# Performance work log

Hardware: AMD Instinct MI355X
Metric: run time of the kernel (lower is better)

The kernel has to match this reference:

```python
import jax, jax.numpy as jnp
import numpy as np

EMBED_DIM = 1024
NUM_HEADS = 16
HEAD_DIM = EMBED_DIM // NUM_HEADS


def setup_inputs() -> dict:
    key = jax.random.key(0)
    ks = jax.random.split(key, 9)
    s = 1.0 / np.sqrt(EMBED_DIM)
    inp = {"x": jax.random.normal(ks[0], (2, 2048, EMBED_DIM), dtype=jnp.float32)}
    for i, name in enumerate(["q", "k", "v", "out"]):
        inp[f"W_{name}"] = jax.random.uniform(ks[1 + 2 * i], (EMBED_DIM, EMBED_DIM), jnp.float32, -s, s)
        inp[f"b_{name}"] = jax.random.uniform(ks[2 + 2 * i], (EMBED_DIM,), jnp.float32, -s, s)
    return inp


def _heads(x):
    # [B, S, D] -> [B, H, S, Dh]
    b, s, _ = x.shape
    return x.reshape(b, s, NUM_HEADS, HEAD_DIM).transpose(0, 2, 1, 3)


def reference(x, W_q, b_q, W_k, b_k, W_v, b_v, W_out, b_out):
    q = _heads(x @ W_q.T + b_q)
    k = _heads(x @ W_k.T + b_k)
    v = _heads(x @ W_v.T + b_v)
    scale = HEAD_DIM ** 0.5
    logits = jnp.einsum("bhqd,bhkd->bhqk", q, k) / scale  # [B,H,S,S]
    s = x.shape[1]
    causal = jnp.tril(jnp.ones((s, s), dtype=bool))
    logits = jnp.where(causal, logits, -jnp.inf)
    a = jax.nn.softmax(logits, axis=-1)
    o = jnp.einsum("bhqk,bhkd->bhqd", a, v)
    o = o.transpose(0, 2, 1, 3).reshape(x.shape[0], s, EMBED_DIM)
    return o @ W_out.T + b_out
```

## Files before the change

kernel.cpp:

```cpp
#include <hip/hip_runtime.h>
#include <hip/hip_bf16.h>

typedef __bf16 bf16_t;
typedef __bf16 bf16x8 __attribute__((ext_vector_type(8)));
typedef __bf16 bf16x4 __attribute__((ext_vector_type(4)));
typedef float  f32x4  __attribute__((ext_vector_type(4)));

#define MFMA16(a, b, c) __builtin_amdgcn_mfma_f32_16x16x32_bf16((a), (b), (c), 0, 0, 0)

constexpr int E  = 1024;
constexpr int S  = 2048;
constexpr int H  = 16;
constexpr int M  = 4096;

__device__ __forceinline__ void glds16(const bf16_t* src, bf16_t* dst) {
  __builtin_amdgcn_global_load_lds(
      (const __attribute__((address_space(1))) void*)src,
      (__attribute__((address_space(3))) void*)dst, 16, 0, 0);
}

template <int ROWS, int NT>
__device__ __forceinline__ void stage_tile(const bf16_t* g, int gld,
                                           bf16_t* lds, int tid) {
  const int w = tid >> 6, l = tid & 63;
#pragma unroll
  for (int i = 0; i < ROWS * 8 / NT; ++i) {
    const int c = i * NT + w * 64 + l;
    const int row = c >> 3;
    const int gch = (c & 7) ^ (row & 7);
    glds16(g + (size_t)row * gld + gch * 8, lds + (size_t)(i * NT + w * 64) * 8);
  }
}

__device__ __forceinline__ bf16x8 read_frag(const bf16_t* lds, int row, int kc) {
  return *(const bf16x8*)(lds + (size_t)((row << 3) + (kc ^ (row & 7))) * 8);
}

__global__ void cvt_all_kernel(const float* __restrict__ x,
                               const float* __restrict__ w0, const float* __restrict__ w1,
                               const float* __restrict__ w2, const float* __restrict__ w3,
                               bf16_t* __restrict__ xb,
                               bf16_t* __restrict__ o0, bf16_t* __restrict__ o1,
                               bf16_t* __restrict__ o2, bf16_t* __restrict__ o3) {
  const int bid = blockIdx.x;
  const float* s;
  bf16_t* d;
  int idx;
  if (bid < 4096) {
    s = x; d = xb; idx = bid * 256 + threadIdx.x;
  } else {
    const int seg = (bid - 4096) >> 10;
    s = seg == 0 ? w0 : seg == 1 ? w1 : seg == 2 ? w2 : w3;
    d = seg == 0 ? o0 : seg == 1 ? o1 : seg == 2 ? o2 : o3;
    idx = ((bid - 4096) & 1023) * 256 + threadIdx.x;
  }
  float4 v = ((const float4*)s)[idx];
  bf16x4 o;
  o[0] = (bf16_t)v.x; o[1] = (bf16_t)v.y; o[2] = (bf16_t)v.z; o[3] = (bf16_t)v.w;
  ((bf16x4*)d)[idx] = o;
}

__global__ __launch_bounds__(512, 2) void qkv8_kernel(
    const bf16_t* __restrict__ xb, const bf16_t* __restrict__ W3,
    const float* __restrict__ bq, const float* __restrict__ bk,
    const float* __restrict__ bv, bf16_t* __restrict__ QKb,
    bf16_t* __restrict__ VT) {
  __shared__ __align__(16) bf16_t As[2][256 * 64];
  __shared__ __align__(16) bf16_t Bs[2][192 * 64];
  const int tid = threadIdx.x;
  const int l = tid & 63, lq = l & 15, qd = l >> 4;
  const int w = tid >> 6, wm = w >> 2, wn = w & 3;

  const int wg = blockIdx.x;
  const int xcd = wg & 7, i5 = wg >> 3;
  const int region = xcd * 2 + (i5 >> 4);
  const int j = i5 & 15;
  const int bx = (region & 3) * 4 + (j & 3);
  const int by = (region >> 2) * 4 + (j >> 2);
  const int m0 = by * 256, n0 = bx * 192;

  const bf16_t* Ag = xb + (size_t)m0 * E;
  const bf16_t* Bg = W3 + (size_t)n0 * E;

  f32x4 acc[8][3];
#pragma unroll
  for (int mi = 0; mi < 8; ++mi)
#pragma unroll
    for (int n = 0; n < 3; ++n) acc[mi][n] = (f32x4){0.f, 0.f, 0.f, 0.f};

  stage_tile<256, 512>(Ag, E, As[0], tid);
  stage_tile<192, 512>(Bg, E, Bs[0], tid);
  __syncthreads();

#pragma unroll 1
  for (int g = 0; g < 16; ++g) {
    const int s = g & 1;
    const bf16_t* Al = As[s];
    const bf16_t* Bl = Bs[s];
    if (g < 15) {
      stage_tile<256, 512>(Ag + (g + 1) * 64, E, As[s ^ 1], tid);
      stage_tile<192, 512>(Bg + (g + 1) * 64, E, Bs[s ^ 1], tid);
    }
#pragma unroll
    for (int kk = 0; kk < 2; ++kk) {
      bf16x8 af[8], bfr[3];
#pragma unroll
      for (int jj = 0; jj < 8; ++jj)
        af[jj] = read_frag(Al, wm * 128 + jj * 16 + lq, kk * 4 + qd);
#pragma unroll
      for (int n = 0; n < 3; ++n)
        bfr[n] = read_frag(Bl, wn * 48 + n * 16 + lq, kk * 4 + qd);
#pragma unroll
      for (int jj = 0; jj < 8; ++jj)
#pragma unroll
        for (int n = 0; n < 3; ++n)
          acc[jj][n] = MFMA16(af[jj], bfr[n], acc[jj][n]);
    }
    __syncthreads();
  }

#pragma unroll
  for (int n = 0; n < 3; ++n) {
    const int col = n0 + wn * 48 + n * 16 + lq;
    const int mat = col >> 10, cc = col & 1023;
    const float bvv = (mat == 0 ? bq : mat == 1 ? bk : bv)[cc];
    if (mat < 2) {
      const float sc = (mat == 0) ? 0.18033688011112043f : 1.0f;
      bf16_t* Out = QKb + (size_t)mat * ((size_t)M * E);
#pragma unroll
      for (int mi = 0; mi < 8; ++mi)
#pragma unroll
        for (int r = 0; r < 4; ++r) {
          const int row = m0 + wm * 128 + mi * 16 + qd * 4 + r;
          Out[(size_t)row * E + cc] = (bf16_t)((acc[mi][n][r] + bvv) * sc);
        }
    } else {
      const int d = cc & 63, hh = cc >> 6;
#pragma unroll
      for (int mi = 0; mi < 8; ++mi) {
        const int row = m0 + wm * 128 + mi * 16 + qd * 4;
        const int bb_ = row >> 11;
        const int s_loc = row & (S - 1);
        const int sl = s_loc & 63, s0 = s_loc & ~63;
        const int a = sl >> 4, b4 = (sl >> 2) & 3;
        const int pb = (a >> 1) * 32 + b4 * 8 + (a & 1) * 4;
        bf16x4 vv;
#pragma unroll
        for (int r = 0; r < 4; ++r) vv[r] = (bf16_t)(acc[mi][n][r] + bvv);
        *(bf16x4*)&VT[((size_t)((bb_ * 16 + hh) * 64 + d)) * S + s0 + pb] = vv;
      }
    }
  }
}

__global__ __launch_bounds__(256) void oproj_gemm_kernel(
    const bf16_t* __restrict__ Ob, const bf16_t* __restrict__ wo,
    const float* __restrict__ bo, float* __restrict__ out) {
  __shared__ __align__(16) bf16_t As[64 * 64];
  __shared__ __align__(16) bf16_t Bs[128 * 64];
  const int tid = threadIdx.x;
  const int n0 = blockIdx.x * 128;
  const int m0 = blockIdx.y * 64;
  const int w = tid >> 6, l = tid & 63, lq = l & 15, qd = l >> 4;
  const int wr = (w >> 1) * 32, wc = (w & 1) * 64;

  f32x4 acc[2][4];
#pragma unroll
  for (int i = 0; i < 2; ++i)
#pragma unroll
    for (int j = 0; j < 4; ++j) acc[i][j] = (f32x4){0.f, 0.f, 0.f, 0.f};

  for (int kt = 0; kt < 16; ++kt) {
    __syncthreads();
    stage_tile<64, 256>(Ob + (size_t)m0 * E + kt * 64, E, As, tid);
    stage_tile<128, 256>(wo + (size_t)n0 * E + kt * 64, E, Bs, tid);
    __syncthreads();
#pragma unroll
    for (int ks = 0; ks < 2; ++ks) {
      bf16x8 af[2], bw[4];
#pragma unroll
      for (int mi = 0; mi < 2; ++mi)
        af[mi] = read_frag(As, wr + mi * 16 + lq, ks * 4 + qd);
#pragma unroll
      for (int ni = 0; ni < 4; ++ni)
        bw[ni] = read_frag(Bs, wc + ni * 16 + lq, ks * 4 + qd);
#pragma unroll
      for (int mi = 0; mi < 2; ++mi)
#pragma unroll
        for (int ni = 0; ni < 4; ++ni)
          acc[mi][ni] = MFMA16(af[mi], bw[ni], acc[mi][ni]);
    }
  }
#pragma unroll
  for (int ni = 0; ni < 4; ++ni) {
    const int col = n0 + wc + ni * 16 + lq;
    const float bvv = bo[col];
#pragma unroll
    for (int mi = 0; mi < 2; ++mi)
#pragma unroll
      for (int r = 0; r < 4; ++r) {
        const int row = m0 + wr + mi * 16 + qd * 4 + r;
        out[(size_t)row * E + col] = acc[mi][ni][r] + bvv;
      }
  }
}

__global__ __launch_bounds__(256, 2) void attn_kernel(
    const bf16_t* __restrict__ Q, const bf16_t* __restrict__ K,
    const bf16_t* __restrict__ VT, bf16_t* __restrict__ O) {
  __shared__ __align__(16) bf16_t Ks[2][64 * 64];
  __shared__ __align__(16) bf16_t Vt[3][64 * 64];

  const int tid = threadIdx.x;
  const int w = tid >> 6, l = tid & 63;
  const int lq = l & 15, qd = l >> 4;
  const int bid = blockIdx.x;
  const int g = bid & 7, t = bid >> 3;
  const int bh = g * 4 + (t & 3);
  const int p = t >> 2;
  const int b = bh >> 4, h = bh & 15;
  const size_t rowbase = (size_t)b * S;
  const bf16_t* Kg = K + rowbase * E + h * 64;
  const bf16_t* Vg = VT + (size_t)bh * 64 * S;

  bf16x8 ones;
#pragma unroll
  for (int j = 0; j < 8; ++j) ones[j] = (bf16_t)1.0f;

  stage_tile<64, 256>(Kg, E, Ks[0], tid);
  stage_tile<64, 256>(Vg, S, Vt[0], tid);
  int cb = 0;
  int vcur = 0;

#pragma unroll 1
  for (int seg = 0; seg < 2; ++seg) {
    const int qt = seg ? p : 31 - p;
    const int qr = qt * 64 + w * 16;

    bf16x8 aq[2];
#pragma unroll
    for (int ks = 0; ks < 2; ++ks)
      aq[ks] = *(const bf16x8*)(Q + (rowbase + qr + lq) * E + h * 64 +
                                ks * 32 + qd * 8);

    f32x4 oacc[4];
#pragma unroll
    for (int nt = 0; nt < 4; ++nt) oacc[nt] = (f32x4){0.f, 0.f, 0.f, 0.f};
    f32x4 osum = (f32x4){0.f, 0.f, 0.f, 0.f};
    bf16x8 ap_prev[2];
    int vprev = vcur;

    auto do_pv = [&](const bf16_t* Vp) {
#pragma unroll
      for (int ks = 0; ks < 2; ++ks) {
        bf16x8 bv[4];
#pragma unroll
        for (int nt = 0; nt < 4; ++nt)
          bv[nt] = read_frag(Vp, nt * 16 + lq, ks * 4 + qd);
#pragma unroll
        for (int nt = 0; nt < 4; ++nt)
          oacc[nt] = MFMA16(ap_prev[ks], bv[nt], oacc[nt]);
        osum = MFMA16(ap_prev[ks], ones, osum);
      }
    };

    for (int kt = 0; kt <= qt; ++kt) {
      __syncthreads();
      const int vnext = (vcur + 1 == 3) ? 0 : vcur + 1;
      if (kt < qt) {
        const int kn = (kt + 1) * 64;
        stage_tile<64, 256>(Kg + (size_t)kn * E, E, Ks[cb ^ 1], tid);
        stage_tile<64, 256>(Vg + kn, S, Vt[vnext], tid);
      } else if (seg == 0) {
        stage_tile<64, 256>(Kg, E, Ks[cb ^ 1], tid);
        stage_tile<64, 256>(Vg, S, Vt[vnext], tid);
      }
      const bf16_t* Kc = Ks[cb];
      const int k0 = kt * 64;
      const bool needmask = (kt == qt);

      f32x4 sacc[4];
#pragma unroll
      for (int nt = 0; nt < 4; ++nt) sacc[nt] = (f32x4){0.f, 0.f, 0.f, 0.f};
      __builtin_amdgcn_s_setprio(1);
#pragma unroll
      for (int ks = 0; ks < 2; ++ks) {
        bf16x8 bk[4];
#pragma unroll
        for (int nt = 0; nt < 4; ++nt)
          bk[nt] = read_frag(Kc, nt * 16 + lq, ks * 4 + qd);
#pragma unroll
        for (int nt = 0; nt < 4; ++nt)
          sacc[nt] = MFMA16(bk[nt], aq[ks], sacc[nt]);
      }
      if (kt > 0) do_pv(Vt[vprev]);
      __builtin_amdgcn_s_setprio(0);

#pragma unroll
      for (int nt = 0; nt < 4; ++nt)
#pragma unroll
        for (int r = 0; r < 4; ++r) {
          float pv = __builtin_amdgcn_exp2f(sacc[nt][r]);
          if (needmask) {
            const int kg = k0 + nt * 16 + qd * 4 + r;
            const int qg = qr + lq;
            pv = (kg > qg) ? 0.f : pv;
          }
          ap_prev[nt >> 1][((nt & 1) << 2) | r] = (bf16_t)pv;
        }
      vprev = vcur;
      vcur = vnext;
      cb ^= 1;
    }
    do_pv(Vt[vprev]);

    float rinv[4];
#pragma unroll
    for (int r = 0; r < 4; ++r) rinv[r] = 1.0f / osum[r];
#pragma unroll
    for (int nt = 0; nt < 4; ++nt)
#pragma unroll
      for (int r = 0; r < 4; ++r) {
        const int qg = qr + qd * 4 + r;
        O[(rowbase + qg) * E + h * 64 + nt * 16 + lq] =
            (bf16_t)(oacc[nt][r] * rinv[r]);
      }
  }
}

extern "C" void kernel_launch(void* const* d_in, const int* in_sizes, int n_in,
                              void* d_out, int out_size, void* d_ws, size_t ws_size,
                              hipStream_t stream) {
  const float* x  = (const float*)d_in[0];
  const float* Wq = (const float*)d_in[1];
  const float* bq = (const float*)d_in[2];
  const float* Wk = (const float*)d_in[3];
  const float* bk = (const float*)d_in[4];
  const float* Wv = (const float*)d_in[5];
  const float* bv = (const float*)d_in[6];
  const float* Wo = (const float*)d_in[7];
  const float* bo = (const float*)d_in[8];
  float* out = (float*)d_out;

  unsigned char* ws = (unsigned char*)d_ws;
  constexpr size_t MB = 1ull << 20;
  bf16_t* xb  = (bf16_t*)(ws + 0 * MB);
  bf16_t* wqb = (bf16_t*)(ws + 8 * MB);
  bf16_t* wkb = (bf16_t*)(ws + 10 * MB);
  bf16_t* wvb = (bf16_t*)(ws + 12 * MB);
  bf16_t* wob = (bf16_t*)(ws + 14 * MB);
  bf16_t* Qb  = (bf16_t*)(ws + 16 * MB);
  bf16_t* VT  = (bf16_t*)(ws + 40 * MB);
  bf16_t* Ob  = xb;

  cvt_all_kernel<<<4096 + 4 * 1024, 256, 0, stream>>>(
      x, Wq, Wk, Wv, Wo, xb, wqb, wkb, wvb, wob);

  qkv8_kernel<<<256, 512, 0, stream>>>(xb, wqb, bq, bk, bv, Qb, VT);

  attn_kernel<<<512, 256, 0, stream>>>(Qb, Qb + (size_t)M * E, VT, Ob);

  oproj_gemm_kernel<<<dim3(8, 64), 256, 0, stream>>>(Ob, wob, bo, out);
}
```

Measured before the change: 174.5 us.

## Restructure QKV GEMM into 256x256 tiles with four-phase interleaved load/MFMA pipeline

The fused QKV projection GEMM now uses 256x256 output tiles over 192 workgroups instead of 256x192 tiles over 256, with one block per CU. The K loop is split into four phases that stage quarter-tiles of the next A/B slices between MFMA bursts, using explicit vmcnt/lgkmcnt waits, raw barriers, sched_barrier and setprio. The goal is to hide global-to-LDS latency behind compute and raise reuse per tile. In exchange occupancy drops to one block per CU, there are more barriers per iteration, and the 192-block grid may leave some CUs idle.

New measurement: 174.1 us. About the same (-0.2%).

```diff
diff --git a/kernel.cpp b/kernel.cpp
--- a/kernel.cpp
+++ b/kernel.cpp
@@ -29,6 +29,21 @@
     const int row = c >> 3;
     const int gch = (c & 7) ^ (row & 7);
     glds16(g + (size_t)row * gld + gch * 8, lds + (size_t)(i * NT + w * 64) * 8);
+  }
+}
+
+__device__ __forceinline__ void stage_A_chunk(const bf16_t* g, int c,
+                                              bf16_t* lds, int tid) {
+  const int w = tid >> 6, l = tid & 63;
+#pragma unroll
+  for (int i = 0; i < 2; ++i) {
+    const int gc = i * 512 + w * 64 + l;
+    const int row_l = gc >> 3;
+    const int col8 = gc & 7;
+    const int h = row_l >> 6, rr = row_l & 63;
+    const int row = h * 128 + c * 64 + rr;
+    const int gch = col8 ^ (row & 7);
+    glds16(g + (size_t)row * E + gch * 8, lds + ((size_t)row * 8 + col8) * 8);
   }
 }
 
@@ -60,85 +75,150 @@
   ((bf16x4*)d)[idx] = o;
 }
 
-__global__ __launch_bounds__(512, 2) void qkv8_kernel(
+__global__ __launch_bounds__(512, 1) void qkv8_kernel(
     const bf16_t* __restrict__ xb, const bf16_t* __restrict__ W3,
     const float* __restrict__ bq, const float* __restrict__ bk,
     const float* __restrict__ bv, bf16_t* __restrict__ QKb,
     bf16_t* __restrict__ VT) {
   __shared__ __align__(16) bf16_t As[2][256 * 64];
-  __shared__ __align__(16) bf16_t Bs[2][192 * 64];
+  __shared__ __align__(16) bf16_t Bs[2][256 * 64];
   const int tid = threadIdx.x;
   const int l = tid & 63, lq = l & 15, qd = l >> 4;
   const int w = tid >> 6, wm = w >> 2, wn = w & 3;
 
-  const int wg = blockIdx.x;
-  const int xcd = wg & 7, i5 = wg >> 3;
-  const int region = xcd * 2 + (i5 >> 4);
-  const int j = i5 & 15;
-  const int bx = (region & 3) * 4 + (j & 3);
-  const int by = (region >> 2) * 4 + (j >> 2);
-  const int m0 = by * 256, n0 = bx * 192;
+  const int swz = (blockIdx.x & 7) * 24 + (blockIdx.x >> 3);
+  const int by = swz / 12, bx = swz % 12;
+  const int m0 = by * 256, n0 = bx * 256;
 
   const bf16_t* Ag = xb + (size_t)m0 * E;
   const bf16_t* Bg = W3 + (size_t)n0 * E;
 
-  f32x4 acc[8][3];
-#pragma unroll
-  for (int mi = 0; mi < 8; ++mi)
-#pragma unroll
-    for (int n = 0; n < 3; ++n) acc[mi][n] = (f32x4){0.f, 0.f, 0.f, 0.f};
-
-  stage_tile<256, 512>(Ag, E, As[0], tid);
-  stage_tile<192, 512>(Bg, E, Bs[0], tid);
-  __syncthreads();
+  f32x4 acc[8][4];
+#pragma unroll
+  for (int jj = 0; jj < 8; ++jj)
+#pragma unroll
+    for (int n = 0; n < 4; ++n) acc[jj][n] = (f32x4){0.f, 0.f, 0.f, 0.f};
+
+  stage_tile<128, 512>(Bg, E, Bs[0], tid);
+  stage_tile<128, 512>(Bg + (size_t)128 * E, E, Bs[0] + 128 * 64, tid);
+  stage_A_chunk(Ag, 0, As[0], tid);
+  stage_A_chunk(Ag, 1, As[0], tid);
+  asm volatile("s_waitcnt vmcnt(2)" ::: "memory");
+  __builtin_amdgcn_s_barrier();
 
 #pragma unroll 1
   for (int g = 0; g < 16; ++g) {
     const int s = g & 1;
     const bf16_t* Al = As[s];
     const bf16_t* Bl = Bs[s];
-    if (g < 15) {
-      stage_tile<256, 512>(Ag + (g + 1) * 64, E, As[s ^ 1], tid);
-      stage_tile<192, 512>(Bg + (g + 1) * 64, E, Bs[s ^ 1], tid);
+    bf16_t* An = As[s ^ 1];
+    bf16_t* Bn = Bs[s ^ 1];
+    const bf16_t* Agn = Ag + (g + 1) * 64;
+    const bf16_t* Bgn = Bg + (g + 1) * 64;
+    const bool more = (g < 15);
+    bf16x8 af[4], bfr[4];
+
+#pragma unroll
+    for (int jj = 0; jj < 4; ++jj)
+      af[jj] = read_frag(Al, wm * 128 + jj * 16 + lq, qd);
+#pragma unroll
+    for (int n = 0; n < 4; ++n)
+      bfr[n] = read_frag(Bl, wn * 64 + n * 16 + lq, qd);
+    if (more) stage_tile<128, 512>(Bgn, E, Bn, tid);
+    __builtin_amdgcn_s_barrier();
+    asm volatile("s_waitcnt lgkmcnt(0)" ::: "memory");
+    __builtin_amdgcn_sched_barrier(0);
+    __builtin_amdgcn_s_setprio(1);
+#pragma unroll
+    for (int jj = 0; jj < 4; ++jj)
+#pragma unroll
+      for (int n = 0; n < 4; ++n)
+        acc[jj][n] = MFMA16(af[jj], bfr[n], acc[jj][n]);
+    __builtin_amdgcn_s_setprio(0);
+    if (more) asm volatile("s_waitcnt vmcnt(2)" ::: "memory");
+    else      asm volatile("s_waitcnt vmcnt(0)" ::: "memory");
+    __builtin_amdgcn_s_barrier();
+
+#pragma unroll
+    for (int jj = 0; jj < 4; ++jj)
+      af[jj] = read_frag(Al, wm * 128 + (4 + jj) * 16 + lq, qd);
+    if (more) stage_tile<128, 512>(Bgn + (size_t)128 * E, E, Bn + 128 * 64, tid);
+    __builtin_amdgcn_s_barrier();
+    asm volatile("s_waitcnt lgkmcnt(0)" ::: "memory");
+    __builtin_amdgcn_sched_barrier(0);
+    __builtin_amdgcn_s_setprio(1);
+#pragma unroll
+    for (int jj = 0; jj < 4; ++jj)
+#pragma unroll
+      for (int n = 0; n < 4; ++n)
+        acc[4 + jj][n] = MFMA16(af[jj], bfr[n], acc[4 + jj][n]);
+    __builtin_amdgcn_s_setprio(0);
+    __builtin_amdgcn_s_barrier();
+
+#pragma unroll
+    for (int jj = 0; jj < 4; ++jj)
+      af[jj] = read_frag(Al, wm * 128 + jj * 16 + lq, 4 + qd);
+#pragma unroll
+    for (int n = 0; n < 4; ++n)
+      bfr[n] = read_frag(Bl, wn * 64 + n * 16 + lq, 4 + qd);
+    if (more) stage_A_chunk(Agn, 0, An, tid);
+    __builtin_amdgcn_s_barrier();
+    asm volatile("s_waitcnt lgkmcnt(0)" ::: "memory");
+    __builtin_amdgcn_sched_barrier(0);
+    __builtin_amdgcn_s_setprio(1);
+#pragma unroll
+    for (int jj = 0; jj < 4; ++jj)
+#pragma unroll
+      for (int n = 0; n < 4; ++n)
+        acc[jj][n] = MFMA16(af[jj], bfr[n], acc[jj][n]);
+    __builtin_amdgcn_s_setprio(0);
+    __builtin_amdgcn_s_barrier();
+
+#pragma unroll
+    for (int jj = 0; jj < 4; ++jj)
+      af[jj] = read_frag(Al, wm * 128 + (4 + jj) * 16 + lq, 4 + qd);
+    if (more) stage_A_chunk(Agn, 1, An, tid);
+    __builtin_amdgcn_s_barrier();
+    asm volatile("s_waitcnt lgkmcnt(0)" ::: "memory");
+    __builtin_amdgcn_sched_barrier(0);
+    __builtin_amdgcn_s_setprio(1);
+#pragma unroll
+    for (int jj = 0; jj < 4; ++jj)
+#pragma unroll
+      for (int n = 0; n < 4; ++n)
+        acc[4 + jj][n] = MFMA16(af[jj], bfr[n], acc[4 + jj][n]);
+    __builtin_amdgcn_s_setprio(0);
+    if (more) asm volatile("s_waitcnt vmcnt(2)" ::: "memory");
+    __builtin_amdgcn_s_barrier();
+  }
+
+  const int mat = n0 >> 10;
+  const int ccb = n0 & 1023;
+  const float* bp = (mat == 0) ? bq : (mat == 1) ? bk : bv;
+  if (mat < 2) {
+    const float sc = (mat == 0) ? 0.18033688011112043f : 1.0f;
+    bf16_t* Out = QKb + (size_t)mat * ((size_t)M * E);
+#pragma unroll
+    for (int n = 0; n < 4; ++n) {
+      const int cc = ccb + wn * 64 + n * 16 + lq;
+      const float bvv = bp[cc];
+#pragma unroll
+      for (int jj = 0; jj < 8; ++jj)
+#pragma unroll
+        for (int r = 0; r < 4; ++r) {
+          const int row = m0 + wm * 128 + jj * 16 + qd * 4 + r;
+          Out[(size_t)row * E + cc] = (bf16_t)((acc[jj][n][r] + bvv) * sc);
+        }
     }
-#pragma unroll
-    for (int kk = 0; kk < 2; ++kk) {
-      bf16x8 af[8], bfr[3];
-#pragma unroll
-      for (int jj = 0; jj < 8; ++jj)
-        af[jj] = read_frag(Al, wm * 128 + jj * 16 + lq, kk * 4 + qd);
-#pragma unroll
-      for (int n = 0; n < 3; ++n)
-        bfr[n] = read_frag(Bl, wn * 48 + n * 16 + lq, kk * 4 + qd);
-#pragma unroll
-      for (int jj = 0; jj < 8; ++jj)
-#pragma unroll
-        for (int n = 0; n < 3; ++n)
-          acc[jj][n] = MFMA16(af[jj], bfr[n], acc[jj][n]);
-    }
-    __syncthreads();
-  }
-
-#pragma unroll
-  for (int n = 0; n < 3; ++n) {
-    const int col = n0 + wn * 48 + n * 16 + lq;
-    const int mat = col >> 10, cc = col & 1023;
-    const float bvv = (mat == 0 ? bq : mat == 1 ? bk : bv)[cc];
-    if (mat < 2) {
-      const float sc = (mat == 0) ? 0.18033688011112043f : 1.0f;
-      bf16_t* Out = QKb + (size_t)mat * ((size_t)M * E);
-#pragma unroll
-      for (int mi = 0; mi < 8; ++mi)
-#pragma unroll
-        for (int r = 0; r < 4; ++r) {
-          const int row = m0 + wm * 128 + mi * 16 + qd * 4 + r;
-          Out[(size_t)row * E + cc] = (bf16_t)((acc[mi][n][r] + bvv) * sc);
-        }
-    } else {
+  } else {
+#pragma unroll
+    for (int n = 0; n < 4; ++n) {
+      const int cc = ccb + wn * 64 + n * 16 + lq;
+      const float bvv = bp[cc];
       const int d = cc & 63, hh = cc >> 6;
 #pragma unroll
-      for (int mi = 0; mi < 8; ++mi) {
-        const int row = m0 + wm * 128 + mi * 16 + qd * 4;
+      for (int jj = 0; jj < 8; ++jj) {
+        const int row = m0 + wm * 128 + jj * 16 + qd * 4;
         const int bb_ = row >> 11;
         const int s_loc = row & (S - 1);
         const int sl = s_loc & 63, s0 = s_loc & ~63;
@@ -146,7 +226,7 @@
         const int pb = (a >> 1) * 32 + b4 * 8 + (a & 1) * 4;
         bf16x4 vv;
 #pragma unroll
-        for (int r = 0; r < 4; ++r) vv[r] = (bf16_t)(acc[mi][n][r] + bvv);
+        for (int r = 0; r < 4; ++r) vv[r] = (bf16_t)(acc[jj][n][r] + bvv);
         *(bf16x4*)&VT[((size_t)((bb_ * 16 + hh) * 64 + d)) * S + s0 + pb] = vv;
       }
     }
@@ -356,7 +436,7 @@
   cvt_all_kernel<<<4096 + 4 * 1024, 256, 0, stream>>>(
       x, Wq, Wk, Wv, Wo, xb, wqb, wkb, wvb, wob);
 
-  qkv8_kernel<<<256, 512, 0, stream>>>(xb, wqb, bq, bk, bv, Qb, VT);
+  qkv8_kernel<<<192, 512, 0, stream>>>(xb, wqb, bq, bk, bv, Qb, VT);
 
   attn_kernel<<<512, 256, 0, stream>>>(Qb, Qb + (size_t)M * E, VT, Ob);
 
```
